# Kernel tuning notes

Hardware: AMD Instinct MI355X
Metric: run time of the kernel (lower is better)

Reference implementation:

```python
import jax, jax.numpy as jnp
import numpy as np

B, NC, CN, K, DN = 2, 256, 256, 16, 64
G, HM, HS, HMOD, MOD_OUT = 8, 128, 128, 64, 5


def setup_inputs() -> dict:
    rng = np.random.default_rng(0)
    # per-neuron top-K neighbors within cell, excluding self, sorted (matches torch buffer build)
    scores = rng.random((NC, CN, CN)).astype(np.float32)
    ii = np.arange(CN)
    scores[:, ii, ii] = -np.inf
    conn = np.argpartition(-scores, K, axis=-1)[..., :K]
    conn = np.sort(conn, axis=-1).astype(np.int32)  # [NC, CN, K]

    key = jax.random.key(0)
    ks = jax.random.split(key, 12)
    n = lambda k, s, sc=1.0: jax.random.normal(k, s, jnp.float32) * sc
    return {
        'h': n(ks[0], (B, NC, CN, DN), 0.01),
        'w_conn': n(ks[1], (B, NC, CN, K), 0.1),
        'cell_context': n(ks[2], (B, NC, DN), 0.1),
        'neuron_id': n(ks[3], (NC, CN, DN), 0.02),
        'msg_w1': n(ks[4], (G, HM, 3 * DN), 0.05), 'msg_b1': jnp.zeros((G, HM)),
        'msg_w2': n(ks[5], (G, DN, HM), 0.005), 'msg_b2': jnp.zeros((G, DN)),
        'state_w1': n(ks[6], (G, HS, 3 * DN), 0.05), 'state_b1': jnp.zeros((G, HS)),
        'state_w2': n(ks[7], (G, DN, HS), 0.005), 'state_b2': jnp.zeros((G, DN)),
        'mod_w1': n(ks[8], (NC, 2 * DN, HMOD), 0.05), 'mod_b1': jnp.zeros((NC, HMOD)),
        'mod_w2': n(ks[9], (NC, HMOD, MOD_OUT), 0.0005), 'mod_b2': jnp.zeros((NC, MOD_OUT)),
        'conn_idx': jnp.asarray(conn),
        'cell_to_group': (jnp.arange(NC) % G).astype(jnp.int32),
    }


def reference(h, w_conn, cell_context, neuron_id,
              msg_w1, msg_b1, msg_w2, msg_b2,
              state_w1, state_b1, state_w2, state_b2,
              mod_w1, mod_b1, mod_w2, mod_b2,
              conn_idx, cell_to_group):
    nc = h.shape[1]
    cell_ix = jnp.arange(nc)[:, None, None]
    # gather K-neighbor states per neuron: [B, NC, CN, K, DN]
    nb = jax.vmap(lambda hb: hb[cell_ix, conn_idx])(h)
    # connection-weighted aggregation
    agg = jnp.einsum('bnck,bnckd->bncd', w_conn, nb)

    g = cell_to_group  # [NC]
    # grouped message MLP (2-layer), per-cell weights gathered from group table
    mfeat = jnp.concatenate([h, agg, jnp.broadcast_to(neuron_id[None], h.shape)], axis=-1)
    mh = jax.nn.gelu(jnp.einsum('bncf,nhf->bnch', mfeat, msg_w1[g]) + msg_b1[g][None, :, None, :])
    msg = jnp.einsum('bnch,ndh->bncd', mh, msg_w2[g]) + msg_b2[g][None, :, None, :]

    # grouped state MLP, residual update on h
    ctx = jnp.broadcast_to(cell_context[:, :, None, :], h.shape)
    sfeat = jnp.concatenate([h, msg, ctx], axis=-1)
    sh = jax.nn.gelu(jnp.einsum('bncf,nhf->bnch', sfeat, state_w1[g]) + state_b1[g][None, :, None, :])
    h_new = h + jnp.einsum('bnch,ndh->bncd', sh, state_w2[g]) + state_b2[g][None, :, None, :]

    # per-cell modulation MLP on pooled stats (h_mean || msg_mean)
    pooled = jnp.concatenate([h_new.mean(axis=2), msg.mean(axis=2)], axis=-1)  # [B, NC, 2DN]
    ph = jax.nn.gelu(jnp.einsum('bnf,nfh->bnh', pooled, mod_w1) + mod_b1[None])
    mod = jnp.einsum('bnh,nho->bno', ph, mod_w2) + mod_b2[None]
    return h_new, msg, mod
```

## Files before the change

### kernel.cpp

```cpp
#include <hip/hip_runtime.h>

#define B_   2
#define NC_  256
#define CN_  256
#define K_   16
#define DN_  64
#define G_   8
#define HM_  128
#define F3_  192

typedef unsigned short u16;
typedef short v8s __attribute__((ext_vector_type(8)));
typedef float v4f __attribute__((ext_vector_type(4)));

#define SMEM_BYTES 149632


__device__ __forceinline__ u16 f2b(float f) {
    unsigned v; __builtin_memcpy(&v, &f, 4);
    v = v + 0x7fffu + ((v >> 16) & 1u);
    return (u16)(v >> 16);
}
__device__ __forceinline__ v8s cvt8(const float* p) {
    float4 a = *(const float4*)p, b = *(const float4*)(p + 4);
    v8s r;
    r[0] = (short)f2b(a.x); r[1] = (short)f2b(a.y); r[2] = (short)f2b(a.z); r[3] = (short)f2b(a.w);
    r[4] = (short)f2b(b.x); r[5] = (short)f2b(b.y); r[6] = (short)f2b(b.z); r[7] = (short)f2b(b.w);
    return r;
}
__device__ __forceinline__ float gelu_t(float x) {
    float u = x * x;
    float t = 1.5957691216057308f * x * __builtin_fmaf(0.044715f, u, 1.0f);
    float e = __expf(-t);
    return x * __builtin_amdgcn_rcpf(1.0f + e);
}

__global__ __launch_bounds__(256) void cvt_w(
    const float* __restrict__ mw1, const float* __restrict__ mw2,
    const float* __restrict__ sw1, const float* __restrict__ sw2,
    u16* __restrict__ dst)
{
    int e = (blockIdx.x * 256 + threadIdx.x) * 4;
    const float* s; int off;
    if      (e < 196608) { s = mw1; off = e; }
    else if (e < 262144) { s = mw2; off = e - 196608; }
    else if (e < 458752) { s = sw1; off = e - 262144; }
    else                 { s = sw2; off = e - 458752; }
    float4 v = *(const float4*)(s + off);
    ushort4 o4;
    o4.x = f2b(v.x); o4.y = f2b(v.y); o4.z = f2b(v.z); o4.w = f2b(v.w);
    *(ushort4*)(dst + e) = o4;
}

__global__ __launch_bounds__(256) void mg_main(
    const float* __restrict__ h,    const float* __restrict__ wconn,
    const float* __restrict__ ctx,  const float* __restrict__ nid,
    const u16* __restrict__ mw1b,   const float* __restrict__ mb1,
    const u16* __restrict__ mw2b,   const float* __restrict__ mb2,
    const u16* __restrict__ sw1b,   const float* __restrict__ sb1,
    const u16* __restrict__ sw2b,   const float* __restrict__ sb2,
    const int* __restrict__ conn,   const int* __restrict__ c2g,
    float* __restrict__ outf,       float* __restrict__ pooled_ws)
{
    const int bn   = blockIdx.x;
    const int n    = bn & 255;
    const int tid  = threadIdx.x;
    const int wave = tid >> 6;
    const int lane = tid & 63;
    const int q    = lane >> 4;
    const int ln   = lane & 15;
    const int g    = c2g[n];

    extern __shared__ char smem[];
    u16*   hT   = (u16*)(smem);
    u16*   big  = (u16*)(smem + 34816);
    u16*   wg   = big;
    u16*   am   = (u16*)(smem + 104448);
    u16*   ctxl = (u16*)(smem + 141312);
    float* hsum = (float*)(smem + 141440);
    float* msum = (float*)(smem + 145536);

    const size_t hbase = (size_t)bn * (CN_ * DN_);
    const size_t nbase = (size_t)n  * (CN_ * DN_);
    float* oH = outf + (size_t)bn * 16384;
    float* oM = outf + (size_t)8388608 + (size_t)bn * 16384;

    if (tid < 64) ctxl[tid] = f2b(ctx[(size_t)bn * DN_ + tid]);
    {
        const float* hrow = h + hbase + (size_t)tid * DN_;
#pragma unroll
        for (int i = 0; i < 16; ++i) {
            float4 v = *(const float4*)(hrow + i * 4);
            hT[(i * 4 + 0) * 272 + tid] = f2b(v.x);
            hT[(i * 4 + 1) * 272 + tid] = f2b(v.y);
            hT[(i * 4 + 2) * 272 + tid] = f2b(v.z);
            hT[(i * 4 + 3) * 272 + tid] = f2b(v.w);
        }
    }
    __syncthreads();

    for (int s = 0; s < 4; ++s) {
#pragma unroll
        for (int i = 0; i < 9; ++i) {
            int idx = tid + i * 256;
            if (idx < 2176) ((uint4*)wg)[idx] = make_uint4(0u, 0u, 0u, 0u);
        }
        __syncthreads();
#pragma unroll
        for (int i = 0; i < 4; ++i) {
            int p  = i * 256 + tid;
            int cl = p >> 4;
            int iv = conn[n * 4096 + s * 1024 + p];
            float wv = wconn[(size_t)bn * 4096 + s * 1024 + p];
            wg[cl * 272 + iv] = f2b(wv);
        }
        __syncthreads();
        {
            v4f a0 = {0,0,0,0}, a1 = {0,0,0,0}, a2 = {0,0,0,0}, a3 = {0,0,0,0};
            const u16* arow = wg + (wave * 16 + ln) * 272 + q * 8;
#pragma unroll
            for (int ks = 0; ks < 8; ++ks) {
                v8s a   = *(const v8s*)(arow + ks * 32);
                v8s bb0 = *(const v8s*)(hT + ( 0 + ln) * 272 + ks * 32 + q * 8);
                v8s bb1 = *(const v8s*)(hT + (16 + ln) * 272 + ks * 32 + q * 8);
                v8s bb2 = *(const v8s*)(hT + (32 + ln) * 272 + ks * 32 + q * 8);
                v8s bb3 = *(const v8s*)(hT + (48 + ln) * 272 + ks * 32 + q * 8);
                a0 = __builtin_amdgcn_mfma_f32_16x16x32_bf16(a, bb0, a0, 0, 0, 0);
                a1 = __builtin_amdgcn_mfma_f32_16x16x32_bf16(a, bb1, a1, 0, 0, 0);
                a2 = __builtin_amdgcn_mfma_f32_16x16x32_bf16(a, bb2, a2, 0, 0, 0);
                a3 = __builtin_amdgcn_mfma_f32_16x16x32_bf16(a, bb3, a3, 0, 0, 0);
            }
            int crow = s * 64 + wave * 16 + q * 4;
#pragma unroll
            for (int r = 0; r < 4; ++r) {
                am[(crow + r) * 72 +  0 + ln] = f2b(a0[r]);
                am[(crow + r) * 72 + 16 + ln] = f2b(a1[r]);
                am[(crow + r) * 72 + 32 + ln] = f2b(a2[r]);
                am[(crow + r) * 72 + 48 + ln] = f2b(a3[r]);
            }
        }
        __syncthreads();
    }

    const int cbase = wave * 64;

    {
        v8s afr[4][6];
#pragma unroll
        for (int mi = 0; mi < 4; ++mi) {
            int c = cbase + mi * 16 + ln;
            afr[mi][0] = cvt8(h + hbase + (size_t)c * 64 +  0 + q * 8);
            afr[mi][1] = cvt8(h + hbase + (size_t)c * 64 + 32 + q * 8);
            afr[mi][2] = *(const v8s*)(am + c * 72 +  0 + q * 8);
            afr[mi][3] = *(const v8s*)(am + c * 72 + 32 + q * 8);
            afr[mi][4] = cvt8(nid + nbase + (size_t)c * 64 +  0 + q * 8);
            afr[mi][5] = cvt8(nid + nbase + (size_t)c * 64 + 32 + q * 8);
        }
        float b1v[8];
#pragma unroll
        for (int nt = 0; nt < 8; ++nt) b1v[nt] = mb1[g * HM_ + nt * 16 + ln];
        const u16* w1g = mw1b + (size_t)g * HM_ * F3_;
#pragma unroll
        for (int nt = 0; nt < 8; ++nt) {
            v4f acc[4] = {{0,0,0,0},{0,0,0,0},{0,0,0,0},{0,0,0,0}};
#pragma unroll
            for (int ks = 0; ks < 6; ++ks) {
                v8s bf = *(const v8s*)(w1g + (nt * 16 + ln) * F3_ + ks * 32 + q * 8);
#pragma unroll
                for (int mi = 0; mi < 4; ++mi)
                    acc[mi] = __builtin_amdgcn_mfma_f32_16x16x32_bf16(afr[mi][ks], bf, acc[mi], 0, 0, 0);
            }
#pragma unroll
            for (int mi = 0; mi < 4; ++mi) {
                int c = cbase + mi * 16 + q * 4;
#pragma unroll
                for (int r = 0; r < 4; ++r)
                    big[(c + r) * 136 + nt * 16 + ln] = f2b(gelu_t(acc[mi][r] + b1v[nt]));
            }
        }
    }

    {
        v8s afr[4][4];
#pragma unroll
        for (int mi = 0; mi < 4; ++mi) {
            int c = cbase + mi * 16 + ln;
#pragma unroll
            for (int ks = 0; ks < 4; ++ks)
                afr[mi][ks] = *(const v8s*)(big + c * 136 + ks * 32 + q * 8);
        }
        const u16* w2g = mw2b + (size_t)g * DN_ * HM_;
        float mpart[4];
#pragma unroll
        for (int nt = 0; nt < 4; ++nt) {
            float bb = mb2[g * DN_ + nt * 16 + ln];
            v4f acc[4] = {{0,0,0,0},{0,0,0,0},{0,0,0,0},{0,0,0,0}};
#pragma unroll
            for (int ks = 0; ks < 4; ++ks) {
                v8s bf = *(const v8s*)(w2g + (nt * 16 + ln) * HM_ + ks * 32 + q * 8);
#pragma unroll
                for (int mi = 0; mi < 4; ++mi)
                    acc[mi] = __builtin_amdgcn_mfma_f32_16x16x32_bf16(afr[mi][ks], bf, acc[mi], 0, 0, 0);
            }
            float ms = 0.0f;
            int d = nt * 16 + ln;
#pragma unroll
            for (int mi = 0; mi < 4; ++mi) {
                int c = cbase + mi * 16 + q * 4;
#pragma unroll
                for (int r = 0; r < 4; ++r) {
                    float mv = acc[mi][r] + bb;
                    am[(c + r) * 72 + d] = f2b(mv);
                    oM[(size_t)(c + r) * 64 + d] = mv;
                    ms += mv;
                }
            }
            mpart[nt] = ms;
        }
#pragma unroll
        for (int nt = 0; nt < 4; ++nt)
            msum[(wave * 4 + q) * 64 + nt * 16 + ln] = mpart[nt];
    }

    {
        v8s cfr0 = *(const v8s*)(ctxl +  0 + q * 8);
        v8s cfr1 = *(const v8s*)(ctxl + 32 + q * 8);
        v8s afr[4][4];
#pragma unroll
        for (int mi = 0; mi < 4; ++mi) {
            int c = cbase + mi * 16 + ln;
            afr[mi][0] = cvt8(h + hbase + (size_t)c * 64 +  0 + q * 8);
            afr[mi][1] = cvt8(h + hbase + (size_t)c * 64 + 32 + q * 8);
            afr[mi][2] = *(const v8s*)(am + c * 72 +  0 + q * 8);
            afr[mi][3] = *(const v8s*)(am + c * 72 + 32 + q * 8);
        }
        float b1v[8];
#pragma unroll
        for (int nt = 0; nt < 8; ++nt) b1v[nt] = sb1[g * HM_ + nt * 16 + ln];
        const u16* w1g = sw1b + (size_t)g * HM_ * F3_;
#pragma unroll
        for (int nt = 0; nt < 8; ++nt) {
            v4f acc[4] = {{0,0,0,0},{0,0,0,0},{0,0,0,0},{0,0,0,0}};
#pragma unroll
            for (int ks = 0; ks < 4; ++ks) {
                v8s bf = *(const v8s*)(w1g + (nt * 16 + ln) * F3_ + ks * 32 + q * 8);
#pragma unroll
                for (int mi = 0; mi < 4; ++mi)
                    acc[mi] = __builtin_amdgcn_mfma_f32_16x16x32_bf16(afr[mi][ks], bf, acc[mi], 0, 0, 0);
            }
#pragma unroll
            for (int ks = 4; ks < 6; ++ks) {
                v8s bf = *(const v8s*)(w1g + (nt * 16 + ln) * F3_ + ks * 32 + q * 8);
                v8s aa = (ks == 4) ? cfr0 : cfr1;
#pragma unroll
                for (int mi = 0; mi < 4; ++mi)
                    acc[mi] = __builtin_amdgcn_mfma_f32_16x16x32_bf16(aa, bf, acc[mi], 0, 0, 0);
            }
#pragma unroll
            for (int mi = 0; mi < 4; ++mi) {
                int c = cbase + mi * 16 + q * 4;
#pragma unroll
                for (int r = 0; r < 4; ++r)
                    big[(c + r) * 136 + nt * 16 + ln] = f2b(gelu_t(acc[mi][r] + b1v[nt]));
            }
        }
    }

    {
        v8s afr[4][4];
#pragma unroll
        for (int mi = 0; mi < 4; ++mi) {
            int c = cbase + mi * 16 + ln;
#pragma unroll
            for (int ks = 0; ks < 4; ++ks)
                afr[mi][ks] = *(const v8s*)(big + c * 136 + ks * 32 + q * 8);
        }
        const u16* w2g = sw2b + (size_t)g * DN_ * HM_;
        float hpart[4];
#pragma unroll
        for (int nt = 0; nt < 4; ++nt) {
            float bb = sb2[g * DN_ + nt * 16 + ln];
            v4f acc[4] = {{0,0,0,0},{0,0,0,0},{0,0,0,0},{0,0,0,0}};
#pragma unroll
            for (int ks = 0; ks < 4; ++ks) {
                v8s bf = *(const v8s*)(w2g + (nt * 16 + ln) * HM_ + ks * 32 + q * 8);
#pragma unroll
                for (int mi = 0; mi < 4; ++mi)
                    acc[mi] = __builtin_amdgcn_mfma_f32_16x16x32_bf16(afr[mi][ks], bf, acc[mi], 0, 0, 0);
            }
            float hs = 0.0f;
            int d = nt * 16 + ln;
#pragma unroll
            for (int mi = 0; mi < 4; ++mi) {
                int c = cbase + mi * 16 + q * 4;
#pragma unroll
                for (int r = 0; r < 4; ++r) {
                    float hv = h[hbase + (size_t)(c + r) * 64 + d];
                    float hn = hv + acc[mi][r] + bb;
                    oH[(size_t)(c + r) * 64 + d] = hn;
                    hs += hn;
                }
            }
            hpart[nt] = hs;
        }
#pragma unroll
        for (int nt = 0; nt < 4; ++nt)
            hsum[(wave * 4 + q) * 64 + nt * 16 + ln] = hpart[nt];
    }
    __syncthreads();

    if (tid < 128) {
        int col = tid & 63;
        const float* src = (tid < 64) ? hsum : msum;
        float s = 0.0f;
#pragma unroll
        for (int i = 0; i < 16; ++i) s += src[i * 64 + col];
        pooled_ws[(size_t)bn * 128 + (tid < 64 ? col : 64 + col)] = s * (1.0f / 256.0f);
    }
}

__global__ __launch_bounds__(64) void mg_mod(
    const float* __restrict__ w1, const float* __restrict__ b1,
    const float* __restrict__ w2, const float* __restrict__ b2,
    const float* __restrict__ pooled, float* __restrict__ outf)
{
    const int bn = blockIdx.x, n = bn & 255, t = threadIdx.x;
    const float* pw = pooled + (size_t)bn * 128;
    float acc = b1[n * 64 + t];
    for (int f = 0; f < 128; ++f)
        acc = __builtin_fmaf(pw[f], w1[(n * 128 + f) * 64 + t], acc);
    float ph = gelu_t(acc);
    float part[5];
#pragma unroll
    for (int o = 0; o < 5; ++o) part[o] = ph * w2[(n * 64 + t) * 5 + o];
#pragma unroll
    for (int off = 32; off > 0; off >>= 1)
#pragma unroll
        for (int o = 0; o < 5; ++o) part[o] += __shfl_down(part[o], off);
    if (t == 0) {
#pragma unroll
        for (int o = 0; o < 5; ++o)
            outf[(size_t)16777216 + bn * 5 + o] = part[o] + b2[n * 5 + o];
    }
}

extern "C" void kernel_launch(void* const* d_in, const int* in_sizes, int n_in,
                              void* d_out, int out_size, void* d_ws, size_t ws_size,
                              hipStream_t stream) {
    const float* h     = (const float*)d_in[0];
    const float* wconn = (const float*)d_in[1];
    const float* ctx   = (const float*)d_in[2];
    const float* nid   = (const float*)d_in[3];
    const float* mw1   = (const float*)d_in[4];
    const float* mb1   = (const float*)d_in[5];
    const float* mw2   = (const float*)d_in[6];
    const float* mb2   = (const float*)d_in[7];
    const float* sw1   = (const float*)d_in[8];
    const float* sb1   = (const float*)d_in[9];
    const float* sw2   = (const float*)d_in[10];
    const float* sb2   = (const float*)d_in[11];
    const float* dw1   = (const float*)d_in[12];
    const float* db1   = (const float*)d_in[13];
    const float* dw2   = (const float*)d_in[14];
    const float* db2   = (const float*)d_in[15];
    const int* conn    = (const int*)d_in[16];
    const int* c2g     = (const int*)d_in[17];
    float* outf  = (float*)d_out;
    u16*   wb    = (u16*)d_ws;
    float* pooled = (float*)((char*)d_ws + 1048576);

    hipFuncSetAttribute(reinterpret_cast<const void*>(&mg_main),
                        hipFuncAttributeMaxDynamicSharedMemorySize, SMEM_BYTES);

    cvt_w<<<512, 256, 0, stream>>>(mw1, mw2, sw1, sw2, wb);
    mg_main<<<512, 256, SMEM_BYTES, stream>>>(h, wconn, ctx, nid,
                                              wb,           mb1,
                                              wb + 196608,  mb2,
                                              wb + 262144,  sb1,
                                              wb + 458752,  sb2,
                                              conn, c2g, outf, pooled);
    mg_mod<<<512, 64, 0, stream>>>(dw1, db1, dw2, db2, pooled, outf);
}
```

Before: 233.8 us.

## Split each cell across two blocks and replace dense gather GEMM with direct aggregation

Each (batch, cell) is now handled by two blocks of 128 neurons each, which halves shared memory per block and allows two blocks per CU across 1024 blocks. The neighbor aggregation drops the zero-filled dense weight matrix and MFMA over all 256 neurons. Each thread instead gathers its 16 neighbor rows from global h in fp32 and accumulates directly, which avoids four rounds of shared-memory clears and barriers. Pooling partials are reduced with shuffles, written per half, and combined in the modulation kernel, which now uses 128 threads. The cost is more scattered global loads of h and some duplicated weight fragment loads across the two blocks.

Measured after the change: 289.8 us. 23.9% more time.

```diff
diff --git a/kernel.cpp b/kernel.cpp
--- a/kernel.cpp
+++ b/kernel.cpp
@@ -12,8 +12,6 @@
 typedef unsigned short u16;
 typedef short v8s __attribute__((ext_vector_type(8)));
 typedef float v4f __attribute__((ext_vector_type(4)));
-
-#define SMEM_BYTES 149632
 
 
 __device__ __forceinline__ u16 f2b(float f) {
@@ -52,7 +50,7 @@
     *(ushort4*)(dst + e) = o4;
 }
 
-__global__ __launch_bounds__(256) void mg_main(
+__global__ __launch_bounds__(256, 2) void mg_main(
     const float* __restrict__ h,    const float* __restrict__ wconn,
     const float* __restrict__ ctx,  const float* __restrict__ nid,
     const u16* __restrict__ mw1b,   const float* __restrict__ mb1,
@@ -60,9 +58,11 @@
     const u16* __restrict__ sw1b,   const float* __restrict__ sb1,
     const u16* __restrict__ sw2b,   const float* __restrict__ sb2,
     const int* __restrict__ conn,   const int* __restrict__ c2g,
-    float* __restrict__ outf,       float* __restrict__ pooled_ws)
+    float* __restrict__ outf,       float* __restrict__ parts)
 {
-    const int bn   = blockIdx.x;
+    const int bid  = blockIdx.x;
+    const int bn   = bid >> 1;
+    const int rh   = bid & 1;
     const int n    = bn & 255;
     const int tid  = threadIdx.x;
     const int wave = tid >> 6;
@@ -71,181 +71,146 @@
     const int ln   = lane & 15;
     const int g    = c2g[n];
 
-    extern __shared__ char smem[];
-    u16*   hT   = (u16*)(smem);
-    u16*   big  = (u16*)(smem + 34816);
-    u16*   wg   = big;
-    u16*   am   = (u16*)(smem + 104448);
-    u16*   ctxl = (u16*)(smem + 141312);
-    float* hsum = (float*)(smem + 141440);
-    float* msum = (float*)(smem + 145536);
+    __shared__ u16   big[128 * 132];
+    __shared__ u16   am [128 * 68];
+    __shared__ float hsumS[4 * 64];
+    __shared__ float msumS[4 * 64];
 
     const size_t hbase = (size_t)bn * (CN_ * DN_);
     const size_t nbase = (size_t)n  * (CN_ * DN_);
     float* oH = outf + (size_t)bn * 16384;
     float* oM = outf + (size_t)8388608 + (size_t)bn * 16384;
 
-    if (tid < 64) ctxl[tid] = f2b(ctx[(size_t)bn * DN_ + tid]);
-    {
-        const float* hrow = h + hbase + (size_t)tid * DN_;
-#pragma unroll
-        for (int i = 0; i < 16; ++i) {
-            float4 v = *(const float4*)(hrow + i * 4);
-            hT[(i * 4 + 0) * 272 + tid] = f2b(v.x);
-            hT[(i * 4 + 1) * 272 + tid] = f2b(v.y);
-            hT[(i * 4 + 2) * 272 + tid] = f2b(v.z);
-            hT[(i * 4 + 3) * 272 + tid] = f2b(v.w);
-        }
-    }
-    __syncthreads();
-
-    for (int s = 0; s < 4; ++s) {
-#pragma unroll
-        for (int i = 0; i < 9; ++i) {
-            int idx = tid + i * 256;
-            if (idx < 2176) ((uint4*)wg)[idx] = make_uint4(0u, 0u, 0u, 0u);
-        }
-        __syncthreads();
-#pragma unroll
-        for (int i = 0; i < 4; ++i) {
-            int p  = i * 256 + tid;
-            int cl = p >> 4;
-            int iv = conn[n * 4096 + s * 1024 + p];
-            float wv = wconn[(size_t)bn * 4096 + s * 1024 + p];
-            wg[cl * 272 + iv] = f2b(wv);
-        }
-        __syncthreads();
-        {
-            v4f a0 = {0,0,0,0}, a1 = {0,0,0,0}, a2 = {0,0,0,0}, a3 = {0,0,0,0};
-            const u16* arow = wg + (wave * 16 + ln) * 272 + q * 8;
-#pragma unroll
-            for (int ks = 0; ks < 8; ++ks) {
-                v8s a   = *(const v8s*)(arow + ks * 32);
-                v8s bb0 = *(const v8s*)(hT + ( 0 + ln) * 272 + ks * 32 + q * 8);
-                v8s bb1 = *(const v8s*)(hT + (16 + ln) * 272 + ks * 32 + q * 8);
-                v8s bb2 = *(const v8s*)(hT + (32 + ln) * 272 + ks * 32 + q * 8);
-                v8s bb3 = *(const v8s*)(hT + (48 + ln) * 272 + ks * 32 + q * 8);
-                a0 = __builtin_amdgcn_mfma_f32_16x16x32_bf16(a, bb0, a0, 0, 0, 0);
-                a1 = __builtin_amdgcn_mfma_f32_16x16x32_bf16(a, bb1, a1, 0, 0, 0);
-                a2 = __builtin_amdgcn_mfma_f32_16x16x32_bf16(a, bb2, a2, 0, 0, 0);
-                a3 = __builtin_amdgcn_mfma_f32_16x16x32_bf16(a, bb3, a3, 0, 0, 0);
-            }
-            int crow = s * 64 + wave * 16 + q * 4;
-#pragma unroll
-            for (int r = 0; r < 4; ++r) {
-                am[(crow + r) * 72 +  0 + ln] = f2b(a0[r]);
-                am[(crow + r) * 72 + 16 + ln] = f2b(a1[r]);
-                am[(crow + r) * 72 + 32 + ln] = f2b(a2[r]);
-                am[(crow + r) * 72 + 48 + ln] = f2b(a3[r]);
-            }
-        }
-        __syncthreads();
-    }
-
-    const int cbase = wave * 64;
-
-    {
-        v8s afr[4][6];
-#pragma unroll
-        for (int mi = 0; mi < 4; ++mi) {
-            int c = cbase + mi * 16 + ln;
-            afr[mi][0] = cvt8(h + hbase + (size_t)c * 64 +  0 + q * 8);
-            afr[mi][1] = cvt8(h + hbase + (size_t)c * 64 + 32 + q * 8);
-            afr[mi][2] = *(const v8s*)(am + c * 72 +  0 + q * 8);
-            afr[mi][3] = *(const v8s*)(am + c * 72 + 32 + q * 8);
-            afr[mi][4] = cvt8(nid + nbase + (size_t)c * 64 +  0 + q * 8);
-            afr[mi][5] = cvt8(nid + nbase + (size_t)c * 64 + 32 + q * 8);
-        }
-        float b1v[8];
-#pragma unroll
-        for (int nt = 0; nt < 8; ++nt) b1v[nt] = mb1[g * HM_ + nt * 16 + ln];
+    {
+        const int c    = tid >> 1;
+        const int gr   = rh * 128 + c;
+        const int d0   = (tid & 1) * 32;
+        const int*   cp = conn  + n * 4096 + gr * 16;
+        const float* wp = wconn + (size_t)bn * 4096 + gr * 16;
+        int   ivv[16]; float wvv[16];
+#pragma unroll
+        for (int k = 0; k < 16; ++k) { ivv[k] = cp[k]; wvv[k] = wp[k]; }
+        float agg[32];
+#pragma unroll
+        for (int j = 0; j < 32; ++j) agg[j] = 0.0f;
+#pragma unroll 4
+        for (int k = 0; k < 16; ++k) {
+            const float* hp = h + hbase + (size_t)ivv[k] * 64 + d0;
+            float w = wvv[k];
+#pragma unroll
+            for (int jj = 0; jj < 8; ++jj) {
+                float4 x = *(const float4*)(hp + jj * 4);
+                agg[jj * 4 + 0] = __builtin_fmaf(w, x.x, agg[jj * 4 + 0]);
+                agg[jj * 4 + 1] = __builtin_fmaf(w, x.y, agg[jj * 4 + 1]);
+                agg[jj * 4 + 2] = __builtin_fmaf(w, x.z, agg[jj * 4 + 2]);
+                agg[jj * 4 + 3] = __builtin_fmaf(w, x.w, agg[jj * 4 + 3]);
+            }
+        }
+        u16* dst = am + c * 68 + d0;
+#pragma unroll
+        for (int j = 0; j < 32; ++j) dst[j] = f2b(agg[j]);
+    }
+
+    const int cbase = wave * 32;
+
+    {
+        v8s afr[2][6];
+#pragma unroll
+        for (int mi = 0; mi < 2; ++mi) {
+            int c  = cbase + mi * 16 + ln;
+            int gc = rh * 128 + c;
+            afr[mi][0] = cvt8(h + hbase + (size_t)gc * 64 +  0 + q * 8);
+            afr[mi][1] = cvt8(h + hbase + (size_t)gc * 64 + 32 + q * 8);
+            afr[mi][2] = *(const v8s*)(am + c * 68 +  0 + q * 8);
+            afr[mi][3] = *(const v8s*)(am + c * 68 + 32 + q * 8);
+            afr[mi][4] = cvt8(nid + nbase + (size_t)gc * 64 +  0 + q * 8);
+            afr[mi][5] = cvt8(nid + nbase + (size_t)gc * 64 + 32 + q * 8);
+        }
         const u16* w1g = mw1b + (size_t)g * HM_ * F3_;
 #pragma unroll
         for (int nt = 0; nt < 8; ++nt) {
-            v4f acc[4] = {{0,0,0,0},{0,0,0,0},{0,0,0,0},{0,0,0,0}};
+            float b1v = mb1[g * HM_ + nt * 16 + ln];
+            v4f acc[2] = {{0,0,0,0},{0,0,0,0}};
 #pragma unroll
             for (int ks = 0; ks < 6; ++ks) {
                 v8s bf = *(const v8s*)(w1g + (nt * 16 + ln) * F3_ + ks * 32 + q * 8);
 #pragma unroll
-                for (int mi = 0; mi < 4; ++mi)
+                for (int mi = 0; mi < 2; ++mi)
                     acc[mi] = __builtin_amdgcn_mfma_f32_16x16x32_bf16(afr[mi][ks], bf, acc[mi], 0, 0, 0);
             }
 #pragma unroll
-            for (int mi = 0; mi < 4; ++mi) {
+            for (int mi = 0; mi < 2; ++mi) {
                 int c = cbase + mi * 16 + q * 4;
 #pragma unroll
                 for (int r = 0; r < 4; ++r)
-                    big[(c + r) * 136 + nt * 16 + ln] = f2b(gelu_t(acc[mi][r] + b1v[nt]));
-            }
-        }
-    }
-
-    {
-        v8s afr[4][4];
-#pragma unroll
-        for (int mi = 0; mi < 4; ++mi) {
+                    big[(c + r) * 132 + nt * 16 + ln] = f2b(gelu_t(acc[mi][r] + b1v));
+            }
+        }
+    }
+
+    {
+        v8s afr[2][4];
+#pragma unroll
+        for (int mi = 0; mi < 2; ++mi) {
             int c = cbase + mi * 16 + ln;
 #pragma unroll
             for (int ks = 0; ks < 4; ++ks)
-                afr[mi][ks] = *(const v8s*)(big + c * 136 + ks * 32 + q * 8);
+                afr[mi][ks] = *(const v8s*)(big + c * 132 + ks * 32 + q * 8);
         }
         const u16* w2g = mw2b + (size_t)g * DN_ * HM_;
-        float mpart[4];
 #pragma unroll
         for (int nt = 0; nt < 4; ++nt) {
             float bb = mb2[g * DN_ + nt * 16 + ln];
-            v4f acc[4] = {{0,0,0,0},{0,0,0,0},{0,0,0,0},{0,0,0,0}};
+            v4f acc[2] = {{0,0,0,0},{0,0,0,0}};
 #pragma unroll
             for (int ks = 0; ks < 4; ++ks) {
                 v8s bf = *(const v8s*)(w2g + (nt * 16 + ln) * HM_ + ks * 32 + q * 8);
 #pragma unroll
-                for (int mi = 0; mi < 4; ++mi)
+                for (int mi = 0; mi < 2; ++mi)
                     acc[mi] = __builtin_amdgcn_mfma_f32_16x16x32_bf16(afr[mi][ks], bf, acc[mi], 0, 0, 0);
             }
             float ms = 0.0f;
             int d = nt * 16 + ln;
 #pragma unroll
-            for (int mi = 0; mi < 4; ++mi) {
+            for (int mi = 0; mi < 2; ++mi) {
                 int c = cbase + mi * 16 + q * 4;
 #pragma unroll
                 for (int r = 0; r < 4; ++r) {
                     float mv = acc[mi][r] + bb;
-                    am[(c + r) * 72 + d] = f2b(mv);
-                    oM[(size_t)(c + r) * 64 + d] = mv;
+                    am[(c + r) * 68 + d] = f2b(mv);
+                    oM[(size_t)(rh * 128 + c + r) * 64 + d] = mv;
                     ms += mv;
                 }
             }
-            mpart[nt] = ms;
-        }
-#pragma unroll
-        for (int nt = 0; nt < 4; ++nt)
-            msum[(wave * 4 + q) * 64 + nt * 16 + ln] = mpart[nt];
-    }
-
-    {
-        v8s cfr0 = *(const v8s*)(ctxl +  0 + q * 8);
-        v8s cfr1 = *(const v8s*)(ctxl + 32 + q * 8);
-        v8s afr[4][4];
-#pragma unroll
-        for (int mi = 0; mi < 4; ++mi) {
-            int c = cbase + mi * 16 + ln;
-            afr[mi][0] = cvt8(h + hbase + (size_t)c * 64 +  0 + q * 8);
-            afr[mi][1] = cvt8(h + hbase + (size_t)c * 64 + 32 + q * 8);
-            afr[mi][2] = *(const v8s*)(am + c * 72 +  0 + q * 8);
-            afr[mi][3] = *(const v8s*)(am + c * 72 + 32 + q * 8);
-        }
-        float b1v[8];
-#pragma unroll
-        for (int nt = 0; nt < 8; ++nt) b1v[nt] = sb1[g * HM_ + nt * 16 + ln];
+            ms += __shfl_xor(ms, 16);
+            ms += __shfl_xor(ms, 32);
+            if (q == 0) msumS[wave * 64 + d] = ms;
+        }
+    }
+
+    {
+        v8s cfr0 = cvt8(ctx + (size_t)bn * DN_ +  0 + q * 8);
+        v8s cfr1 = cvt8(ctx + (size_t)bn * DN_ + 32 + q * 8);
+        v8s afr[2][4];
+#pragma unroll
+        for (int mi = 0; mi < 2; ++mi) {
+            int c  = cbase + mi * 16 + ln;
+            int gc = rh * 128 + c;
+            afr[mi][0] = cvt8(h + hbase + (size_t)gc * 64 +  0 + q * 8);
+            afr[mi][1] = cvt8(h + hbase + (size_t)gc * 64 + 32 + q * 8);
+            afr[mi][2] = *(const v8s*)(am + c * 68 +  0 + q * 8);
+            afr[mi][3] = *(const v8s*)(am + c * 68 + 32 + q * 8);
+        }
         const u16* w1g = sw1b + (size_t)g * HM_ * F3_;
 #pragma unroll
         for (int nt = 0; nt < 8; ++nt) {
-            v4f acc[4] = {{0,0,0,0},{0,0,0,0},{0,0,0,0},{0,0,0,0}};
+            float b1v = sb1[g * HM_ + nt * 16 + ln];
+            v4f acc[2] = {{0,0,0,0},{0,0,0,0}};
 #pragma unroll
             for (int ks = 0; ks < 4; ++ks) {
                 v8s bf = *(const v8s*)(w1g + (nt * 16 + ln) * F3_ + ks * 32 + q * 8);
 #pragma unroll
-                for (int mi = 0; mi < 4; ++mi)
+                for (int mi = 0; mi < 2; ++mi)
                     acc[mi] = __builtin_amdgcn_mfma_f32_16x16x32_bf16(afr[mi][ks], bf, acc[mi], 0, 0, 0);
             }
 #pragma unroll
@@ -253,94 +218,100 @@
                 v8s bf = *(const v8s*)(w1g + (nt * 16 + ln) * F3_ + ks * 32 + q * 8);
                 v8s aa = (ks == 4) ? cfr0 : cfr1;
 #pragma unroll
-                for (int mi = 0; mi < 4; ++mi)
+                for (int mi = 0; mi < 2; ++mi)
                     acc[mi] = __builtin_amdgcn_mfma_f32_16x16x32_bf16(aa, bf, acc[mi], 0, 0, 0);
             }
 #pragma unroll
-            for (int mi = 0; mi < 4; ++mi) {
+            for (int mi = 0; mi < 2; ++mi) {
                 int c = cbase + mi * 16 + q * 4;
 #pragma unroll
                 for (int r = 0; r < 4; ++r)
-                    big[(c + r) * 136 + nt * 16 + ln] = f2b(gelu_t(acc[mi][r] + b1v[nt]));
-            }
-        }
-    }
-
-    {
-        v8s afr[4][4];
-#pragma unroll
-        for (int mi = 0; mi < 4; ++mi) {
+                    big[(c + r) * 132 + nt * 16 + ln] = f2b(gelu_t(acc[mi][r] + b1v));
+            }
+        }
+    }
+
+    {
+        v8s afr[2][4];
+#pragma unroll
+        for (int mi = 0; mi < 2; ++mi) {
             int c = cbase + mi * 16 + ln;
 #pragma unroll
             for (int ks = 0; ks < 4; ++ks)
-                afr[mi][ks] = *(const v8s*)(big + c * 136 + ks * 32 + q * 8);
+                afr[mi][ks] = *(const v8s*)(big + c * 132 + ks * 32 + q * 8);
         }
         const u16* w2g = sw2b + (size_t)g * DN_ * HM_;
-        float hpart[4];
 #pragma unroll
         for (int nt = 0; nt < 4; ++nt) {
             float bb = sb2[g * DN_ + nt * 16 + ln];
-            v4f acc[4] = {{0,0,0,0},{0,0,0,0},{0,0,0,0},{0,0,0,0}};
+            v4f acc[2] = {{0,0,0,0},{0,0,0,0}};
 #pragma unroll
             for (int ks = 0; ks < 4; ++ks) {
                 v8s bf = *(const v8s*)(w2g + (nt * 16 + ln) * HM_ + ks * 32 + q * 8);
 #pragma unroll
-                for (int mi = 0; mi < 4; ++mi)
+                for (int mi = 0; mi < 2; ++mi)
                     acc[mi] = __builtin_amdgcn_mfma_f32_16x16x32_bf16(afr[mi][ks], bf, acc[mi], 0, 0, 0);
             }
             float hs = 0.0f;
             int d = nt * 16 + ln;
 #pragma unroll
-            for (int mi = 0; mi < 4; ++mi) {
+            for (int mi = 0; mi < 2; ++mi) {
                 int c = cbase + mi * 16 + q * 4;
 #pragma unroll
                 for (int r = 0; r < 4; ++r) {
-                    float hv = h[hbase + (size_t)(c + r) * 64 + d];
+                    int gc = rh * 128 + c + r;
+                    float hv = h[hbase + (size_t)gc * 64 + d];
                     float hn = hv + acc[mi][r] + bb;
-                    oH[(size_t)(c + r) * 64 + d] = hn;
+                    oH[(size_t)gc * 64 + d] = hn;
                     hs += hn;
                 }
             }
-            hpart[nt] = hs;
-        }
-#pragma unroll
-        for (int nt = 0; nt < 4; ++nt)
-            hsum[(wave * 4 + q) * 64 + nt * 16 + ln] = hpart[nt];
+            hs += __shfl_xor(hs, 16);
+            hs += __shfl_xor(hs, 32);
+            if (q == 0) hsumS[wave * 64 + d] = hs;
+        }
     }
     __syncthreads();
 
     if (tid < 128) {
         int col = tid & 63;
-        const float* src = (tid < 64) ? hsum : msum;
-        float s = 0.0f;
-#pragma unroll
-        for (int i = 0; i < 16; ++i) s += src[i * 64 + col];
-        pooled_ws[(size_t)bn * 128 + (tid < 64 ? col : 64 + col)] = s * (1.0f / 256.0f);
-    }
-}
-
-__global__ __launch_bounds__(64) void mg_mod(
+        const float* src = (tid < 64) ? hsumS : msumS;
+        float s = src[0 * 64 + col] + src[1 * 64 + col] + src[2 * 64 + col] + src[3 * 64 + col];
+        parts[(size_t)bn * 256 + rh * 128 + (tid < 64 ? col : 64 + col)] = s;
+    }
+}
+
+__global__ __launch_bounds__(128) void mg_mod(
     const float* __restrict__ w1, const float* __restrict__ b1,
     const float* __restrict__ w2, const float* __restrict__ b2,
-    const float* __restrict__ pooled, float* __restrict__ outf)
+    const float* __restrict__ parts, float* __restrict__ outf)
 {
     const int bn = blockIdx.x, n = bn & 255, t = threadIdx.x;
-    const float* pw = pooled + (size_t)bn * 128;
-    float acc = b1[n * 64 + t];
-    for (int f = 0; f < 128; ++f)
-        acc = __builtin_fmaf(pw[f], w1[(n * 128 + f) * 64 + t], acc);
-    float ph = gelu_t(acc);
-    float part[5];
-#pragma unroll
-    for (int o = 0; o < 5; ++o) part[o] = ph * w2[(n * 64 + t) * 5 + o];
-#pragma unroll
-    for (int off = 32; off > 0; off >>= 1)
-#pragma unroll
-        for (int o = 0; o < 5; ++o) part[o] += __shfl_down(part[o], off);
-    if (t == 0) {
-#pragma unroll
-        for (int o = 0; o < 5; ++o)
-            outf[(size_t)16777216 + bn * 5 + o] = part[o] + b2[n * 5 + o];
+    const int col = t & 63, fh = t >> 6;
+    const float* pr = parts + (size_t)bn * 256;
+    __shared__ float r1[64];
+
+    float acc = (fh == 0) ? b1[n * 64 + col] : 0.0f;
+    for (int f = fh * 64; f < fh * 64 + 64; ++f) {
+        float pv = (pr[f] + pr[128 + f]) * (1.0f / 256.0f);
+        acc = __builtin_fmaf(pv, w1[(n * 128 + f) * 64 + col], acc);
+    }
+    if (fh == 1) r1[col] = acc;
+    __syncthreads();
+    if (fh == 0) {
+        float ph = gelu_t(acc + r1[col]);
+        float part[5];
+#pragma unroll
+        for (int o = 0; o < 5; ++o) part[o] = ph * w2[(n * 64 + col) * 5 + o];
+#pragma unroll
+        for (int off = 32; off > 0; off >>= 1)
+#pragma unroll
+            for (int o = 0; o < 5; ++o) part[o] += __shfl_down(part[o], off);
+        if (col == 0) {
+#pragma unroll
+            for (int o = 0; o < 5; ++o)
+                outf[(size_t)16777216 + bn * 5 + o] = part[o] + b2[n * 5 + o];
+        }
     }
 }
 
@@ -367,17 +338,14 @@
     const int* c2g     = (const int*)d_in[17];
     float* outf  = (float*)d_out;
     u16*   wb    = (u16*)d_ws;
-    float* pooled = (float*)((char*)d_ws + 1048576);
-
-    hipFuncSetAttribute(reinterpret_cast<const void*>(&mg_main),
-                        hipFuncAttributeMaxDynamicSharedMemorySize, SMEM_BYTES);
+    float* parts = (float*)((char*)d_ws + 1048576);
 
     cvt_w<<<512, 256, 0, stream>>>(mw1, mw2, sw1, sw2, wb);
-    mg_main<<<512, 256, SMEM_BYTES, stream>>>(h, wconn, ctx, nid,
-                                              wb,           mb1,
-                                              wb + 196608,  mb2,
-                                              wb + 262144,  sb1,
-                                              wb + 458752,  sb2,
-                                              conn, c2g, outf, pooled);
-    mg_mod<<<512, 64, 0, stream>>>(dw1, db1, dw2, db2, pooled, outf);
-}
+    mg_main<<<1024, 256, 0, stream>>>(h, wconn, ctx, nid,
+                                      wb,           mb1,
+                                      wb + 196608,  mb2,
+                                      wb + 262144,  sb1,
+                                      wb + 458752,  sb2,
+                                      conn, c2g, outf, parts);
+    mg_mod<<<512, 128, 0, stream>>>(dw1, db1, dw2, db2, parts, outf);
+}
```
